# Optimization experiments

Hardware: AMD Instinct MI355X
Metric: run time of the kernel (lower is better)

## Reference

```python
import jax, jax.numpy as jnp
import numpy as np

L, B = 512, 1024
K = 64
IN, OBS, ST = 32, 32, 32


def setup_inputs() -> dict:
    key = jax.random.key(0)
    ks = iter(jax.random.split(key, 64))
    def W(o, i):
        return (jax.random.normal(next(ks), (o, i), jnp.float32) / np.sqrt(i)).astype(jnp.float32)
    def b(o):
        return (jax.random.normal(next(ks), (o,), jnp.float32) * 0.01).astype(jnp.float32)
    return dict(
        external_input_seq=jax.random.normal(next(ks), (L, B, IN), jnp.float32),
        observations_seq=jax.random.normal(next(ks), (L, B, OBS), jnp.float32),
        eps=jax.random.normal(next(ks), (L, B, ST), jnp.float32),
        pu_W1=W(K, IN), pu_b1=b(K), pu_W2=W(K, K), pu_b2=b(K),
        px_W1=W(K, OBS), px_b1=b(K), px_W2=W(K, K), px_b2=b(K),
        pz_W1=W(K, ST), pz_b1=b(K), pz_W2=W(K, K), pz_b2=b(K),
        post_W1=W(K, K), post_b1=b(K), post_W2=W(K, K), post_b2=b(K),
        post_Wmu=W(ST, K), post_bmu=b(ST), post_Wls=W(ST, K), post_bls=b(ST),
        inf_Wih=W(3 * K, K), inf_Whh=W(3 * K, K), inf_bih=b(3 * K), inf_bhh=b(3 * K),
        gen_Wih=W(3 * K, 2 * K), gen_Whh=W(3 * K, K), gen_bih=b(3 * K), gen_bhh=b(3 * K),
    )


def _preprocess(x, W1, b1, W2, b2):
    # PreProcess: two Linear+ReLU layers
    t = jax.nn.relu(x @ W1.T + b1)
    return jax.nn.relu(t @ W2.T + b2)


def _dblock(x, W1, b1, W2, b2, Wmu, bmu, Wls, bls):
    # DBlock_Relu: gated hidden t = relu(fc1(x)) * sigmoid(fc2(x)); heads mu, logsigma
    t = jax.nn.relu(x @ W1.T + b1) * jax.nn.sigmoid(x @ W2.T + b2)
    return x @ jnp.zeros((0,))[None, :0].T if False else (t @ Wmu.T + bmu, t @ Wls.T + bls)


def _gru(xs, h0, Wih, Whh, bih, bhh):
    # torch.nn.GRU gate order: reset, update, new
    def step(h, x):
        gi = x @ Wih.T + bih
        gh = h @ Whh.T + bhh
        i_r, i_z, i_n = jnp.split(gi, 3, axis=-1)
        h_r, h_z, h_n = jnp.split(gh, 3, axis=-1)
        r = jax.nn.sigmoid(i_r + h_r)
        z = jax.nn.sigmoid(i_z + h_z)
        n = jnp.tanh(i_n + r * h_n)
        h_new = (1.0 - z) * n + z * h
        return h_new, h_new
    return jax.lax.scan(step, h0, xs)


def reference(external_input_seq, observations_seq, eps,
              pu_W1, pu_b1, pu_W2, pu_b2,
              px_W1, px_b1, px_W2, px_b2,
              pz_W1, pz_b1, pz_W2, pz_b2,
              post_W1, post_b1, post_W2, post_b2,
              post_Wmu, post_bmu, post_Wls, post_bls,
              inf_Wih, inf_Whh, inf_bih, inf_bhh,
              gen_Wih, gen_Whh, gen_bih, gen_bhh):
    l, batch, _ = external_input_seq.shape
    k = inf_Whh.shape[1]
    h0 = jnp.zeros((batch, k), external_input_seq.dtype)

    u_emb = _preprocess(external_input_seq, pu_W1, pu_b1, pu_W2, pu_b2)   # [l,b,k]
    x_emb = _preprocess(observations_seq, px_W1, px_b1, px_W2, px_b2)     # [l,b,k]

    _, d_seq = _gru(x_emb, h0, inf_Wih, inf_Whh, inf_bih, inf_bhh)        # [l,b,k]

    # posterior q(z_t | d_t) — depends only on d_seq, so fully vectorized over time
    z_mu, z_logsigma = _dblock(d_seq, post_W1, post_b1, post_W2, post_b2,
                               post_Wmu, post_bmu, post_Wls, post_bls)
    sampled_state = z_mu + jnp.exp(0.5 * z_logsigma) * eps               # reparam sample

    z_emb = _preprocess(sampled_state, pz_W1, pz_b1, pz_W2, pz_b2)        # [l,b,k]
    gen_in = jnp.concatenate([z_emb, u_emb], axis=-1)                     # [l,b,2k]
    hn, h_all = _gru(gen_in, h0, gen_Wih, gen_Whh, gen_bih, gen_bhh)
    # h_seq in original is [h0, h1, ..., h_{l-1}] (drops last)
    h_seq = jnp.concatenate([h0[None], h_all[:-1]], axis=0)

    return (z_mu, z_logsigma, sampled_state, h_seq, x_emb, hn)
```

## Files before the change

kernel.cpp:

```cpp
#include <hip/hip_runtime.h>

#define L_T 512
#define BATCH 1024
#define LB (L_T*BATCH)
#define NT (LB/64)

typedef short bf16x8 __attribute__((ext_vector_type(8)));
typedef float f32x4 __attribute__((ext_vector_type(4)));
typedef unsigned short u16;

#define MFMA_B16(a,b,c) __builtin_amdgcn_mfma_f32_16x16x32_bf16((a),(b),(c),0,0,0)

__device__ __forceinline__ short f2bs(float f){
  union{float f; unsigned u;} c; c.f=f;
  unsigned r = (c.u + 0x7FFFu + ((c.u>>16)&1u)) >> 16;
  return (short)r;
}

__device__ __forceinline__ unsigned cvtpk(float lo, float hi){
  unsigned d;
  asm("v_cvt_pk_bf16_f32 %0, %1, %2" : "=v"(d) : "v"(lo), "v"(hi));
  return d;
}

__device__ __forceinline__ float fsig(float x){
  return __builtin_amdgcn_rcpf(1.0f + __expf(-x));
}
__device__ __forceinline__ float ftanh(float x){
  return 1.0f - 2.0f*__builtin_amdgcn_rcpf(1.0f + __expf(2.0f*x));
}

__device__ __forceinline__ void store8(u16* d, float4 a, float4 b){
  bf16x8 v;
  v[0]=f2bs(a.x); v[1]=f2bs(a.y); v[2]=f2bs(a.z); v[3]=f2bs(a.w);
  v[4]=f2bs(b.x); v[5]=f2bs(b.y); v[6]=f2bs(b.z); v[7]=f2bs(b.w);
  *(bf16x8*)d = v;
}

__device__ __forceinline__ bf16x8 bfrag_f32(const float* p){
  float4 a = *(const float4*)p;
  float4 b = *(const float4*)(p+4);
  bf16x8 v;
  v[0]=f2bs(a.x); v[1]=f2bs(a.y); v[2]=f2bs(a.z); v[3]=f2bs(a.w);
  v[4]=f2bs(b.x); v[5]=f2bs(b.y); v[6]=f2bs(b.z); v[7]=f2bs(b.w);
  return v;
}

__device__ __forceinline__ void dma16(const void* g, void* l){
  __builtin_amdgcn_global_load_lds(
      (const __attribute__((address_space(1))) void*)g,
      (__attribute__((address_space(3))) void*)l, 16, 0, 0);
}

__device__ __forceinline__ void pre_body(
    int bid,
    const float* __restrict__ src, const float* __restrict__ W1,
    const float* __restrict__ b1, const float* __restrict__ W2,
    const float* __restrict__ b2,
    u16* __restrict__ out_b16, int ostride, int ooff,
    float* __restrict__ out_f32)
{
  __shared__ u16 in_t[64*40];
  __shared__ u16 w1t[64*40];
  __shared__ u16 w2t[64*88];
  __shared__ u16 t1t[64*88];
  __shared__ float lb1[64], lb2[64];

  const int t = threadIdx.x;
  const size_t row0 = (size_t)bid * 64;

  {
    int r = t>>2, q = t&3;
    const float* ps = src + (row0 + r)*32 + q*8;
    store8(in_t + r*40 + q*8, *(const float4*)ps, *(const float4*)(ps+4));
    const float* pw = W1 + r*32 + q*8;
    store8(w1t + r*40 + q*8, *(const float4*)pw, *(const float4*)(pw+4));
    const float* pw2 = W2 + r*64 + q*16;
    store8(w2t + r*88 + q*16,     *(const float4*)pw2,     *(const float4*)(pw2+4));
    store8(w2t + r*88 + q*16 + 8, *(const float4*)(pw2+8), *(const float4*)(pw2+12));
    if (t < 64) lb1[t] = b1[t];
    else if (t < 128) lb2[t-64] = b2[t-64];
  }
  __syncthreads();

  const int lane = t & 63, wave = t >> 6;
  const int l15 = lane & 15, l4 = lane >> 4;
  const int rs = wave*16;

  {
    bf16x8 a = *(const bf16x8*)(in_t + (rs + l15)*40 + l4*8);
    #pragma unroll
    for (int ct = 0; ct < 4; ++ct) {
      f32x4 acc = {0.f,0.f,0.f,0.f};
      bf16x8 bw = *(const bf16x8*)(w1t + (ct*16 + l15)*40 + l4*8);
      acc = MFMA_B16(a, bw, acc);
      float bias = lb1[ct*16 + l15];
      #pragma unroll
      for (int i = 0; i < 4; ++i) {
        float v = fmaxf(acc[i] + bias, 0.f);
        t1t[(rs + l4*4 + i)*88 + ct*16 + l15] = (u16)f2bs(v);
      }
    }
  }
  __syncthreads();

  {
    bf16x8 a0 = *(const bf16x8*)(t1t + (rs + l15)*88 + l4*8);
    bf16x8 a1 = *(const bf16x8*)(t1t + (rs + l15)*88 + 32 + l4*8);
    #pragma unroll
    for (int ct = 0; ct < 4; ++ct) {
      f32x4 acc = {0.f,0.f,0.f,0.f};
      bf16x8 b0 = *(const bf16x8*)(w2t + (ct*16 + l15)*88 + l4*8);
      bf16x8 b1v = *(const bf16x8*)(w2t + (ct*16 + l15)*88 + 32 + l4*8);
      acc = MFMA_B16(a0, b0, acc);
      acc = MFMA_B16(a1, b1v, acc);
      float bias = lb2[ct*16 + l15];
      #pragma unroll
      for (int i = 0; i < 4; ++i) {
        float v = fmaxf(acc[i] + bias, 0.f);
        size_t gr = row0 + rs + l4*4 + i;
        int col = ct*16 + l15;
        if (out_b16) out_b16[gr*(size_t)ostride + ooff + col] = (u16)f2bs(v);
        if (out_f32) out_f32[gr*64 + col] = v;
      }
    }
  }
}

__global__ __launch_bounds__(256) void k_pre2(
    const float* __restrict__ obs,
    const float* __restrict__ pxW1, const float* __restrict__ pxb1,
    const float* __restrict__ pxW2, const float* __restrict__ pxb2,
    u16* __restrict__ xemb16, float* __restrict__ xembf32,
    const float* __restrict__ ext,
    const float* __restrict__ puW1, const float* __restrict__ pub1,
    const float* __restrict__ puW2, const float* __restrict__ pub2,
    u16* __restrict__ gen_in)
{
  int bid = blockIdx.x;
  if (bid < NT) pre_body(bid, obs, pxW1, pxb1, pxW2, pxb2, xemb16, 64, 0, xembf32);
  else          pre_body(bid - NT, ext, puW1, pub1, puW2, pub2, gen_in, 128, 64, nullptr);
}


#define SMEM_U16 39552
#define M_DT   0
#define M_W1T  5632
#define M_W2T  11264
#define M_TT   16896
#define M_ZW2T 22528
#define M_ZW1T 28160
#define M_ST   30720
#define M_WMUT 33280
#define M_WLST 36096
#define M_BIAS 38912

__device__ void inf_phase(
    int P, u16* smem,
    const u16* __restrict__ xin,
    const float* __restrict__ Wih, const float* __restrict__ Whh,
    const float* __restrict__ bih, const float* __restrict__ bhh,
    u16* __restrict__ dseq_out,
    float* __restrict__ hstate)
{
  u16* xchunk = smem;
  u16* ht     = smem + 16384;

  const int t = threadIdx.x;
  const int lane = t & 63, wave = t >> 6;
  const int l15 = lane & 15, l4 = lane >> 4;
  const int b0 = blockIdx.x * 16;
  const int kcol = wave*16 + l15;
  const int c0   = wave*16 + l4*4;

  bf16x8 wihf[3][2], whhf[3][2];
  #pragma unroll
  for (int g = 0; g < 3; ++g) {
    int grow = g*64 + kcol;
    #pragma unroll
    for (int kc = 0; kc < 2; ++kc) {
      wihf[g][kc] = bfrag_f32(Wih + (size_t)grow*64 + kc*32 + l4*8);
      whhf[g][kc] = bfrag_f32(Whh + (size_t)grow*64 + kc*32 + l4*8);
    }
  }
  f32x4 bv0, bv1, bvi, bvh;
  #pragma unroll
  for (int i = 0; i < 4; ++i) {
    bv0[i] = bih[c0+i]      + bhh[c0+i];
    bv1[i] = bih[64+c0+i]   + bhh[64+c0+i];
    bvi[i] = bih[128+c0+i];
    bvh[i] = bhh[128+c0+i];
  }

  auto issue_chunk = [&](int gc, int bufi){
    const size_t step0 = (size_t)gc*8;
    u16* dst0 = xchunk + bufi*8192;
    #pragma unroll
    for (int j = 0; j < 4; ++j) {
      int o = (j*4 + wave)*1024;
      int slot = o/16 + lane;
      int r_all = slot >> 3;
      int q = slot & 7;
      int slice = r_all >> 4, r = r_all & 15;
      int qs = q ^ (r & 7);
      const u16* g = xin + ((step0 + slice)*BATCH + b0 + r)*64 + qs*8;
      dma16(g, dst0 + o/2);
    }
  };

  float h[4];
  if (P == 0) { h[0]=h[1]=h[2]=h[3]=0.f; }
  else {
    float4 hv = *(const float4*)(hstate + (size_t)(b0 + l15)*64 + c0);
    h[0]=hv.x; h[1]=hv.y; h[2]=hv.z; h[3]=hv.w;
  }

  f32x4 gp0, gp1, gp2;
  issue_chunk(P*8, 0);

  for (int cc = 0; cc < 8; ++cc) {
    const int gc = P*8 + cc;
    const int cb = cc & 1;
    const u16* xbuf = xchunk + cb*8192;
    #pragma unroll
    for (int sp = 0; sp < 8; ++sp) {
      const int step = gc*8 + sp;

      {
        uint2 pv; pv.x = cvtpk(h[0], h[1]); pv.y = cvtpk(h[2], h[3]);
        *(uint2*)(ht + (sp&1)*1152 + l15*72 + c0) = pv;
      }

      if (sp == 0) asm volatile("s_waitcnt vmcnt(0)" ::: "memory");
      asm volatile("s_waitcnt lgkmcnt(0)\n\ts_barrier" ::: "memory");

      const u16* htr = ht + (sp&1)*1152 + l15*72;
      bf16x8 ha0 = *(const bf16x8*)(htr + l4*8);
      bf16x8 ha1 = *(const bf16x8*)(htr + 32 + l4*8);

      f32x4 a0, a1, a2;
      if (sp == 0) {
        const u16* xb = xbuf + l15*64;
        bf16x8 xa[2];
        #pragma unroll
        for (int kc = 0; kc < 2; ++kc)
          xa[kc] = *(const bf16x8*)(xb + (((l4 + 4*kc) ^ (l15 & 7)) * 8));
        a0 = bv0; a1 = bv1; a2 = bvi;
        #pragma unroll
        for (int kc = 0; kc < 2; ++kc) {
          a0 = MFMA_B16(wihf[0][kc], xa[kc], a0);
          a1 = MFMA_B16(wihf[1][kc], xa[kc], a1);
          a2 = MFMA_B16(wihf[2][kc], xa[kc], a2);
        }
      } else {
        a0 = gp0; a1 = gp1; a2 = gp2;
      }

      if (sp == 1 && cc + 1 < 8) issue_chunk(gc + 1, cb ^ 1);

      f32x4 g0 = MFMA_B16(whhf[0][0], ha0, a0);
      g0       = MFMA_B16(whhf[0][1], ha1, g0);
      f32x4 g1 = MFMA_B16(whhf[1][0], ha0, a1);
      g1       = MFMA_B16(whhf[1][1], ha1, g1);
      f32x4 gn = MFMA_B16(whhf[2][0], ha0, bvh);
      gn       = MFMA_B16(whhf[2][1], ha1, gn);

      if (sp < 7) {
        const u16* xb = xbuf + (sp+1)*1024 + l15*64;
        bf16x8 xn[2];
        #pragma unroll
        for (int kc = 0; kc < 2; ++kc)
          xn[kc] = *(const bf16x8*)(xb + (((l4 + 4*kc) ^ (l15 & 7)) * 8));
        gp0 = bv0; gp1 = bv1; gp2 = bvi;
        #pragma unroll
        for (int kc = 0; kc < 2; ++kc) {
          gp0 = MFMA_B16(wihf[0][kc], xn[kc], gp0);
          gp1 = MFMA_B16(wihf[1][kc], xn[kc], gp1);
          gp2 = MFMA_B16(wihf[2][kc], xn[kc], gp2);
        }
      }

      #pragma unroll
      for (int i = 0; i < 4; ++i) {
        float r = fsig(g0[i]);
        float z = fsig(g1[i]);
        float n = ftanh(a2[i] + r*gn[i]);
        h[i] = z*(h[i] - n) + n;
      }

      {
        uint2 dv; dv.x = cvtpk(h[0], h[1]); dv.y = cvtpk(h[2], h[3]);
        *(uint2*)(dseq_out + ((size_t)step*BATCH + b0 + l15)*64 + c0) = dv;
      }
    }
  }

  float4 hv; hv.x=h[0]; hv.y=h[1]; hv.z=h[2]; hv.w=h[3];
  *(float4*)(hstate + (size_t)(b0 + l15)*64 + c0) = hv;
}

__device__ void gen_phase(
    int P, u16* smem,
    const u16* __restrict__ xin,
    const float* __restrict__ Wih, const float* __restrict__ Whh,
    const float* __restrict__ bih, const float* __restrict__ bhh,
    float* __restrict__ hseq,
    float* __restrict__ hstate)
{
  u16* xchunk = smem;
  u16* ht     = smem + 32768;

  const int t = threadIdx.x;
  const int lane = t & 63, wave = t >> 6;
  const int l15 = lane & 15, l4 = lane >> 4;
  const int b0 = (blockIdx.x - 64) * 16;
  const int kcol = wave*16 + l15;
  const int c0   = wave*16 + l4*4;

  bf16x8 wihf[3][4], whhf[3][2];
  #pragma unroll
  for (int g = 0; g < 3; ++g) {
    int grow = g*64 + kcol;
    #pragma unroll
    for (int kc = 0; kc < 4; ++kc)
      wihf[g][kc] = bfrag_f32(Wih + (size_t)grow*128 + kc*32 + l4*8);
    #pragma unroll
    for (int kc = 0; kc < 2; ++kc)
      whhf[g][kc] = bfrag_f32(Whh + (size_t)grow*64 + kc*32 + l4*8);
  }
  f32x4 bv0, bv1, bvi, bvh;
  #pragma unroll
  for (int i = 0; i < 4; ++i) {
    bv0[i] = bih[c0+i]      + bhh[c0+i];
    bv1[i] = bih[64+c0+i]   + bhh[64+c0+i];
    bvi[i] = bih[128+c0+i];
    bvh[i] = bhh[128+c0+i];
  }

  auto issue_chunk = [&](int gc, int bufi){
    const size_t step0 = (size_t)gc*8;
    u16* dst0 = xchunk + bufi*16384;
    #pragma unroll
    for (int j = 0; j < 8; ++j) {
      int o = (j*4 + wave)*1024;
      int slot = o/16 + lane;
      int r_all = slot >> 4;
      int q = slot & 15;
      int slice = r_all >> 4, r = r_all & 15;
      int qs = q ^ (r & 7);
      const u16* g = xin + ((step0 + slice)*BATCH + b0 + r)*128 + qs*8;
      dma16(g, dst0 + o/2);
    }
  };

  float h[4];
  if (P == 2) { h[0]=h[1]=h[2]=h[3]=0.f; }
  else {
    float4 hv = *(const float4*)(hstate + (size_t)(b0 + l15)*64 + c0);
    h[0]=hv.x; h[1]=hv.y; h[2]=hv.z; h[3]=hv.w;
  }

  const int C0 = (P - 2) * 8;
  f32x4 gp0, gp1, gp2;
  issue_chunk(C0, 0);

  for (int cc = 0; cc < 8; ++cc) {
    const int gc = C0 + cc;
    const int cb = cc & 1;
    const u16* xbuf = xchunk + cb*16384;
    #pragma unroll
    for (int sp = 0; sp < 8; ++sp) {
      const int step = gc*8 + sp;

      {
        uint2 pv; pv.x = cvtpk(h[0], h[1]); pv.y = cvtpk(h[2], h[3]);
        *(uint2*)(ht + (sp&1)*1152 + l15*72 + c0) = pv;
        float4 hv; hv.x=h[0]; hv.y=h[1]; hv.z=h[2]; hv.w=h[3];
        *(float4*)(hseq + ((size_t)step*BATCH + b0 + l15)*64 + c0) = hv;
      }

      if (sp == 0) asm volatile("s_waitcnt vmcnt(0)" ::: "memory");
      asm volatile("s_waitcnt lgkmcnt(0)\n\ts_barrier" ::: "memory");

      const u16* htr = ht + (sp&1)*1152 + l15*72;
      bf16x8 ha0 = *(const bf16x8*)(htr + l4*8);
      bf16x8 ha1 = *(const bf16x8*)(htr + 32 + l4*8);

      f32x4 a0, a1, a2;
      if (sp == 0) {
        const u16* xb = xbuf + l15*128;
        bf16x8 xa[4];
        #pragma unroll
        for (int kc = 0; kc < 4; ++kc)
          xa[kc] = *(const bf16x8*)(xb + (((l4 + 4*kc) ^ (l15 & 7)) * 8));
        a0 = bv0; a1 = bv1; a2 = bvi;
        #pragma unroll
        for (int kc = 0; kc < 4; ++kc) {
          a0 = MFMA_B16(wihf[0][kc], xa[kc], a0);
          a1 = MFMA_B16(wihf[1][kc], xa[kc], a1);
          a2 = MFMA_B16(wihf[2][kc], xa[kc], a2);
        }
      } else {
        a0 = gp0; a1 = gp1; a2 = gp2;
      }

      if (sp == 1 && cc + 1 < 8) issue_chunk(gc + 1, cb ^ 1);

      f32x4 g0 = MFMA_B16(whhf[0][0], ha0, a0);
      g0       = MFMA_B16(whhf[0][1], ha1, g0);
      f32x4 g1 = MFMA_B16(whhf[1][0], ha0, a1);
      g1       = MFMA_B16(whhf[1][1], ha1, g1);
      f32x4 gn = MFMA_B16(whhf[2][0], ha0, bvh);
      gn       = MFMA_B16(whhf[2][1], ha1, gn);

      if (sp < 7) {
        const u16* xb = xbuf + (sp+1)*2048 + l15*128;
        bf16x8 xn[4];
        #pragma unroll
        for (int kc = 0; kc < 4; ++kc)
          xn[kc] = *(const bf16x8*)(xb + (((l4 + 4*kc) ^ (l15 & 7)) * 8));
        gp0 = bv0; gp1 = bv1; gp2 = bvi;
        #pragma unroll
        for (int kc = 0; kc < 4; ++kc) {
          gp0 = MFMA_B16(wihf[0][kc], xn[kc], gp0);
          gp1 = MFMA_B16(wihf[1][kc], xn[kc], gp1);
          gp2 = MFMA_B16(wihf[2][kc], xn[kc], gp2);
        }
      }

      #pragma unroll
      for (int i = 0; i < 4; ++i) {
        float r = fsig(g0[i]);
        float z = fsig(g1[i]);
        float n = ftanh(a2[i] + r*gn[i]);
        h[i] = z*(h[i] - n) + n;
      }
    }
  }

  float4 hv; hv.x=h[0]; hv.y=h[1]; hv.z=h[2]; hv.w=h[3];
  *(float4*)(hstate + (size_t)(b0 + l15)*64 + c0) = hv;
}

__device__ void mid_phase(
    int P, u16* smem,
    const u16* __restrict__ dseq,
    const float* __restrict__ eps,
    const float* __restrict__ W1, const float* __restrict__ b1,
    const float* __restrict__ W2, const float* __restrict__ b2,
    const float* __restrict__ Wmu, const float* __restrict__ bmu,
    const float* __restrict__ Wls, const float* __restrict__ bls,
    const float* __restrict__ zW1, const float* __restrict__ zb1,
    const float* __restrict__ zW2, const float* __restrict__ zb2,
    float* __restrict__ out_mu, float* __restrict__ out_ls, float* __restrict__ out_s,
    u16* __restrict__ gen_in)
{
  u16* dt   = smem + M_DT;
  u16* w1t  = smem + M_W1T;
  u16* w2t  = smem + M_W2T;
  u16* tt   = smem + M_TT;
  u16* zw2t = smem + M_ZW2T;
  u16* zw1t = smem + M_ZW1T;
  u16* st   = smem + M_ST;
  u16* wmut = smem + M_WMUT;
  u16* wlst = smem + M_WLST;
  float* fb = (float*)(smem + M_BIAS);
  float* lb1 = fb, *lb2 = fb+64, *lbz1 = fb+128, *lbz2 = fb+192;
  float* lbmu = fb+256, *lbls = fb+288;

  const int t = threadIdx.x;

  {
    int r = t>>2, q = t&3;
    const float* p1 = W1 + r*64 + q*16;
    store8(w1t + r*88 + q*16,     *(const float4*)p1,     *(const float4*)(p1+4));
    store8(w1t + r*88 + q*16 + 8, *(const float4*)(p1+8), *(const float4*)(p1+12));
    const float* p2 = W2 + r*64 + q*16;
    store8(w2t + r*88 + q*16,     *(const float4*)p2,     *(const float4*)(p2+4));
    store8(w2t + r*88 + q*16 + 8, *(const float4*)(p2+8), *(const float4*)(p2+12));
    const float* pz2 = zW2 + r*64 + q*16;
    store8(zw2t + r*88 + q*16,     *(const float4*)pz2,     *(const float4*)(pz2+4));
    store8(zw2t + r*88 + q*16 + 8, *(const float4*)(pz2+8), *(const float4*)(pz2+12));
    const float* pz1 = zW1 + r*32 + q*8;
    store8(zw1t + r*40 + q*8, *(const float4*)pz1, *(const float4*)(pz1+4));
    if (t < 128) {
      int r2 = t>>2, q2 = t&3;
      const float* pm = Wmu + r2*64 + q2*16;
      store8(wmut + r2*88 + q2*16,     *(const float4*)pm,     *(const float4*)(pm+4));
      store8(wmut + r2*88 + q2*16 + 8, *(const float4*)(pm+8), *(const float4*)(pm+12));
    } else {
      int t2 = t - 128; int r2 = t2>>2, q2 = t2&3;
      const float* pl = Wls + r2*64 + q2*16;
      store8(wlst + r2*88 + q2*16,     *(const float4*)pl,     *(const float4*)(pl+4));
      store8(wlst + r2*88 + q2*16 + 8, *(const float4*)(pl+8), *(const float4*)(pl+12));
    }
    if (t < 64) { lb1[t] = b1[t]; lbz1[t] = zb1[t]; }
    else if (t < 128) { lb2[t-64] = b2[t-64]; lbz2[t-64] = zb2[t-64]; }
    else if (t < 160) lbmu[t-128] = bmu[t-128];
    else if (t < 192) lbls[t-160] = bls[t-160];
  }

  const int lane = t & 63, wave = t >> 6;
  const int l15 = lane & 15, l4 = lane >> 4;
  const int rs = wave*16;
  const int bidm = blockIdx.x - 128;
  const size_t t0 = (size_t)(P - 1) * 64;

  for (int j = 0; j < 8; ++j) {
    const size_t row0 = t0*BATCH + ((size_t)bidm*8 + j)*64;

    __syncthreads();
    {
      int r = t>>2, q = t&3;
      const u16* pd = dseq + (row0 + r)*64 + q*16;
      *(bf16x8*)(dt + r*88 + q*16)     = *(const bf16x8*)pd;
      *(bf16x8*)(dt + r*88 + q*16 + 8) = *(const bf16x8*)(pd + 8);
    }
    __syncthreads();

    {
      bf16x8 a0 = *(const bf16x8*)(dt + (rs + l15)*88 + l4*8);
      bf16x8 a1 = *(const bf16x8*)(dt + (rs + l15)*88 + 32 + l4*8);
      #pragma unroll
      for (int ct = 0; ct < 4; ++ct) {
        f32x4 c1 = {0.f,0.f,0.f,0.f}, c2 = {0.f,0.f,0.f,0.f};
        bf16x8 w1a = *(const bf16x8*)(w1t + (ct*16 + l15)*88 + l4*8);
        bf16x8 w1b = *(const bf16x8*)(w1t + (ct*16 + l15)*88 + 32 + l4*8);
        bf16x8 w2a = *(const bf16x8*)(w2t + (ct*16 + l15)*88 + l4*8);
        bf16x8 w2b = *(const bf16x8*)(w2t + (ct*16 + l15)*88 + 32 + l4*8);
        c1 = MFMA_B16(a0, w1a, c1); c1 = MFMA_B16(a1, w1b, c1);
        c2 = MFMA_B16(a0, w2a, c2); c2 = MFMA_B16(a1, w2b, c2);
        float bb1 = lb1[ct*16 + l15], bb2 = lb2[ct*16 + l15];
        #pragma unroll
        for (int i = 0; i < 4; ++i) {
          float tv = fmaxf(c1[i] + bb1, 0.f) * fsig(c2[i] + bb2);
          tt[(rs + l4*4 + i)*88 + ct*16 + l15] = (u16)f2bs(tv);
        }
      }
    }
    __syncthreads();

    {
      bf16x8 a0 = *(const bf16x8*)(tt + (rs + l15)*88 + l4*8);
      bf16x8 a1 = *(const bf16x8*)(tt + (rs + l15)*88 + 32 + l4*8);
      #pragma unroll
      for (int ct = 0; ct < 2; ++ct) {
        f32x4 cmu = {0.f,0.f,0.f,0.f}, cls = {0.f,0.f,0.f,0.f};
        bf16x8 wma = *(const bf16x8*)(wmut + (ct*16 + l15)*88 + l4*8);
        bf16x8 wmb = *(const bf16x8*)(wmut + (ct*16 + l15)*88 + 32 + l4*8);
        bf16x8 wla = *(const bf16x8*)(wlst + (ct*16 + l15)*88 + l4*8);
        bf16x8 wlb = *(const bf16x8*)(wlst + (ct*16 + l15)*88 + 32 + l4*8);
        cmu = MFMA_B16(a0, wma, cmu); cmu = MFMA_B16(a1, wmb, cmu);
        cls = MFMA_B16(a0, wla, cls); cls = MFMA_B16(a1, wlb, cls);
        float bm = lbmu[ct*16 + l15], bl = lbls[ct*16 + l15];
        #pragma unroll
        for (int i = 0; i < 4; ++i) {
          size_t R = row0 + rs + l4*4 + i;
          int col = ct*16 + l15;
          float mu = cmu[i] + bm;
          float ls = cls[i] + bl;
          float e  = eps[R*32 + col];
          float s  = mu + __expf(0.5f*ls)*e;
          out_mu[R*32 + col] = mu;
          out_ls[R*32 + col] = ls;
          out_s [R*32 + col] = s;
          st[(rs + l4*4 + i)*40 + col] = (u16)f2bs(s);
        }
      }
    }
    __syncthreads();

    {
      bf16x8 a = *(const bf16x8*)(st + (rs + l15)*40 + l4*8);
      #pragma unroll
      for (int ct = 0; ct < 4; ++ct) {
        f32x4 acc = {0.f,0.f,0.f,0.f};
        bf16x8 bw = *(const bf16x8*)(zw1t + (ct*16 + l15)*40 + l4*8);
        acc = MFMA_B16(a, bw, acc);
        float bias = lbz1[ct*16 + l15];
        #pragma unroll
        for (int i = 0; i < 4; ++i) {
          float v = fmaxf(acc[i] + bias, 0.f);
          dt[(rs + l4*4 + i)*88 + ct*16 + l15] = (u16)f2bs(v);
        }
      }
    }
    __syncthreads();

    {
      bf16x8 a0 = *(const bf16x8*)(dt + (rs + l15)*88 + l4*8);
      bf16x8 a1 = *(const bf16x8*)(dt + (rs + l15)*88 + 32 + l4*8);
      #pragma unroll
      for (int ct = 0; ct < 4; ++ct) {
        f32x4 acc = {0.f,0.f,0.f,0.f};
        bf16x8 b0 = *(const bf16x8*)(zw2t + (ct*16 + l15)*88 + l4*8);
        bf16x8 b1v = *(const bf16x8*)(zw2t + (ct*16 + l15)*88 + 32 + l4*8);
        acc = MFMA_B16(a0, b0, acc);
        acc = MFMA_B16(a1, b1v, acc);
        float bias = lbz2[ct*16 + l15];
        #pragma unroll
        for (int i = 0; i < 4; ++i) {
          float v = fmaxf(acc[i] + bias, 0.f);
          size_t gr = row0 + rs + l4*4 + i;
          gen_in[gr*128 + ct*16 + l15] = (u16)f2bs(v);
        }
      }
    }
  }
}

__global__ __launch_bounds__(256, 1) void k_phase(
    int P,
    const u16* xemb16, u16* gen_in,
    const float* eps,
    const float* iWih, const float* iWhh, const float* ibih, const float* ibhh,
    const float* gWih, const float* gWhh, const float* gbih, const float* gbhh,
    const float* poW1, const float* pob1, const float* poW2, const float* pob2,
    const float* poWmu, const float* pobmu, const float* poWls, const float* pobls,
    const float* pzW1, const float* pzb1, const float* pzW2, const float* pzb2,
    u16* dseq, float* out_mu, float* out_ls, float* out_s,
    float* hseq, float* hn, float* hstate_inf)
{
  __shared__ u16 smem[SMEM_U16];
  const int bid = blockIdx.x;
  if (bid < 64) {
    if (P < 8)
      inf_phase(P, smem, xemb16, iWih, iWhh, ibih, ibhh, dseq, hstate_inf);
  } else if (bid < 128) {
    if (P >= 2)
      gen_phase(P, smem, gen_in, gWih, gWhh, gbih, gbhh, hseq, hn);
  } else {
    if (P >= 1 && P <= 8)
      mid_phase(P, smem, dseq, eps, poW1, pob1, poW2, pob2,
                poWmu, pobmu, poWls, pobls, pzW1, pzb1, pzW2, pzb2,
                out_mu, out_ls, out_s, gen_in);
  }
}


extern "C" void kernel_launch(void* const* d_in, const int* in_sizes, int n_in,
                              void* d_out, int out_size, void* d_ws, size_t ws_size,
                              hipStream_t stream) {
  const float* ext  = (const float*)d_in[0];
  const float* obs  = (const float*)d_in[1];
  const float* eps  = (const float*)d_in[2];
  const float* puW1 = (const float*)d_in[3];  const float* pub1 = (const float*)d_in[4];
  const float* puW2 = (const float*)d_in[5];  const float* pub2 = (const float*)d_in[6];
  const float* pxW1 = (const float*)d_in[7];  const float* pxb1 = (const float*)d_in[8];
  const float* pxW2 = (const float*)d_in[9];  const float* pxb2 = (const float*)d_in[10];
  const float* pzW1 = (const float*)d_in[11]; const float* pzb1 = (const float*)d_in[12];
  const float* pzW2 = (const float*)d_in[13]; const float* pzb2 = (const float*)d_in[14];
  const float* poW1 = (const float*)d_in[15]; const float* pob1 = (const float*)d_in[16];
  const float* poW2 = (const float*)d_in[17]; const float* pob2 = (const float*)d_in[18];
  const float* poWmu= (const float*)d_in[19]; const float* pobmu= (const float*)d_in[20];
  const float* poWls= (const float*)d_in[21]; const float* pobls= (const float*)d_in[22];
  const float* iWih = (const float*)d_in[23]; const float* iWhh = (const float*)d_in[24];
  const float* ibih = (const float*)d_in[25]; const float* ibhh = (const float*)d_in[26];
  const float* gWih = (const float*)d_in[27]; const float* gWhh = (const float*)d_in[28];
  const float* gbih = (const float*)d_in[29]; const float* gbhh = (const float*)d_in[30];

  float* out = (float*)d_out;
  const size_t OFF_MU   = 0;
  const size_t OFF_LS   = (size_t)LB*32;
  const size_t OFF_S    = (size_t)LB*64;
  const size_t OFF_HSEQ = (size_t)LB*96;
  const size_t OFF_XEMB = (size_t)LB*96 + (size_t)LB*64;
  const size_t OFF_HN   = OFF_XEMB + (size_t)LB*64;

  u16* gen_in = (u16*)d_ws;
  u16* dseq   = (u16*)(out + OFF_MU);
  u16* xemb16 = (u16*)(out + OFF_HSEQ + (size_t)LB*32);
  float* hstate_inf = out + OFF_S + (size_t)LB*32 - 65536;

  k_pre2<<<2*NT, 256, 0, stream>>>(obs, pxW1, pxb1, pxW2, pxb2, xemb16, out + OFF_XEMB,
                                   ext, puW1, pub1, puW2, pub2, gen_in);
  for (int P = 0; P < 10; ++P) {
    k_phase<<<256, 256, 0, stream>>>(P, xemb16, gen_in, eps,
                                     iWih, iWhh, ibih, ibhh,
                                     gWih, gWhh, gbih, gbhh,
                                     poW1, pob1, poW2, pob2,
                                     poWmu, pobmu, poWls, pobls,
                                     pzW1, pzb1, pzW2, pzb2,
                                     dseq, out + OFF_MU, out + OFF_LS, out + OFF_S,
                                     out + OFF_HSEQ, out + OFF_HN, hstate_inf);
  }
}
```

Measured before the change: 485.3 us.

## Overlap input preprocessing with recurrent phases by deferring tiles to mid blocks

```diff
diff --git a/kernel.cpp b/kernel.cpp
--- a/kernel.cpp
+++ b/kernel.cpp
@@ -52,22 +52,40 @@
       (__attribute__((address_space(3))) void*)l, 16, 0, 0);
 }
 
-__device__ __forceinline__ void pre_body(
-    int bid,
+#define SMEM_U16 39552
+#define M_DT   0
+#define M_W1T  5632
+#define M_W2T  11264
+#define M_TT   16896
+#define M_ZW2T 22528
+#define M_ZW1T 28160
+#define M_ST   30720
+#define M_WMUT 33280
+#define M_WLST 36096
+#define M_BIAS 38912
+#define PT_IN   0
+#define PT_W1   2560
+#define PT_W2   5120
+#define PT_T1   10752
+#define PT_BIAS 16384
+
+__device__ void pre_tile(
+    u16* smem, size_t row0,
     const float* __restrict__ src, const float* __restrict__ W1,
     const float* __restrict__ b1, const float* __restrict__ W2,
     const float* __restrict__ b2,
     u16* __restrict__ out_b16, int ostride, int ooff,
     float* __restrict__ out_f32)
 {
-  __shared__ u16 in_t[64*40];
-  __shared__ u16 w1t[64*40];
-  __shared__ u16 w2t[64*88];
-  __shared__ u16 t1t[64*88];
-  __shared__ float lb1[64], lb2[64];
+  u16* in_t = smem + PT_IN;
+  u16* w1t  = smem + PT_W1;
+  u16* w2t  = smem + PT_W2;
+  u16* t1t  = smem + PT_T1;
+  float* lb1 = (float*)(smem + PT_BIAS);
+  float* lb2 = lb1 + 64;
 
   const int t = threadIdx.x;
-  const size_t row0 = (size_t)bid * 64;
+  __syncthreads();
 
   {
     int r = t>>2, q = t&3;
@@ -120,14 +138,14 @@
         float v = fmaxf(acc[i] + bias, 0.f);
         size_t gr = row0 + rs + l4*4 + i;
         int col = ct*16 + l15;
-        if (out_b16) out_b16[gr*(size_t)ostride + ooff + col] = (u16)f2bs(v);
+        out_b16[gr*(size_t)ostride + ooff + col] = (u16)f2bs(v);
         if (out_f32) out_f32[gr*64 + col] = v;
       }
     }
   }
 }
 
-__global__ __launch_bounds__(256) void k_pre2(
+__global__ __launch_bounds__(256) void k_pre_small(
     const float* __restrict__ obs,
     const float* __restrict__ pxW1, const float* __restrict__ pxb1,
     const float* __restrict__ pxW2, const float* __restrict__ pxb2,
@@ -137,23 +155,16 @@
     const float* __restrict__ puW2, const float* __restrict__ pub2,
     u16* __restrict__ gen_in)
 {
+  __shared__ u16 smem[16640];
   int bid = blockIdx.x;
-  if (bid < NT) pre_body(bid, obs, pxW1, pxb1, pxW2, pxb2, xemb16, 64, 0, xembf32);
-  else          pre_body(bid - NT, ext, puW1, pub1, puW2, pub2, gen_in, 128, 64, nullptr);
-}
-
-
-#define SMEM_U16 39552
-#define M_DT   0
-#define M_W1T  5632
-#define M_W2T  11264
-#define M_TT   16896
-#define M_ZW2T 22528
-#define M_ZW1T 28160
-#define M_ST   30720
-#define M_WMUT 33280
-#define M_WLST 36096
-#define M_BIAS 38912
+  if (bid < 2048)
+    pre_tile(smem, (size_t)bid*64, obs, pxW1, pxb1, pxW2, pxb2,
+             xemb16, 64, 0, xembf32);
+  else
+    pre_tile(smem, (size_t)(bid-2048)*64, ext, puW1, pub1, puW2, pub2,
+             gen_in, 128, 64, nullptr);
+}
+
 
 __device__ void inf_phase(
     int P, u16* smem,
@@ -453,165 +464,189 @@
     const float* __restrict__ zW1, const float* __restrict__ zb1,
     const float* __restrict__ zW2, const float* __restrict__ zb2,
     float* __restrict__ out_mu, float* __restrict__ out_ls, float* __restrict__ out_s,
-    u16* __restrict__ gen_in)
+    u16* __restrict__ gen_in,
+    const float* __restrict__ obs,
+    const float* __restrict__ pxW1, const float* __restrict__ pxb1,
+    const float* __restrict__ pxW2, const float* __restrict__ pxb2,
+    u16* __restrict__ xemb16, float* __restrict__ xembf32,
+    const float* __restrict__ ext,
+    const float* __restrict__ puW1, const float* __restrict__ pub1,
+    const float* __restrict__ puW2, const float* __restrict__ pub2)
 {
-  u16* dt   = smem + M_DT;
-  u16* w1t  = smem + M_W1T;
-  u16* w2t  = smem + M_W2T;
-  u16* tt   = smem + M_TT;
-  u16* zw2t = smem + M_ZW2T;
-  u16* zw1t = smem + M_ZW1T;
-  u16* st   = smem + M_ST;
-  u16* wmut = smem + M_WMUT;
-  u16* wlst = smem + M_WLST;
-  float* fb = (float*)(smem + M_BIAS);
-  float* lb1 = fb, *lb2 = fb+64, *lbz1 = fb+128, *lbz2 = fb+192;
-  float* lbmu = fb+256, *lbls = fb+288;
-
   const int t = threadIdx.x;
-
-  {
-    int r = t>>2, q = t&3;
-    const float* p1 = W1 + r*64 + q*16;
-    store8(w1t + r*88 + q*16,     *(const float4*)p1,     *(const float4*)(p1+4));
-    store8(w1t + r*88 + q*16 + 8, *(const float4*)(p1+8), *(const float4*)(p1+12));
-    const float* p2 = W2 + r*64 + q*16;
-    store8(w2t + r*88 + q*16,     *(const float4*)p2,     *(const float4*)(p2+4));
-    store8(w2t + r*88 + q*16 + 8, *(const float4*)(p2+8), *(const float4*)(p2+12));
-    const float* pz2 = zW2 + r*64 + q*16;
-    store8(zw2t + r*88 + q*16,     *(const float4*)pz2,     *(const float4*)(pz2+4));
-    store8(zw2t + r*88 + q*16 + 8, *(const float4*)(pz2+8), *(const float4*)(pz2+12));
-    const float* pz1 = zW1 + r*32 + q*8;
-    store8(zw1t + r*40 + q*8, *(const float4*)pz1, *(const float4*)(pz1+4));
-    if (t < 128) {
-      int r2 = t>>2, q2 = t&3;
-      const float* pm = Wmu + r2*64 + q2*16;
-      store8(wmut + r2*88 + q2*16,     *(const float4*)pm,     *(const float4*)(pm+4));
-      store8(wmut + r2*88 + q2*16 + 8, *(const float4*)(pm+8), *(const float4*)(pm+12));
-    } else {
-      int t2 = t - 128; int r2 = t2>>2, q2 = t2&3;
-      const float* pl = Wls + r2*64 + q2*16;
-      store8(wlst + r2*88 + q2*16,     *(const float4*)pl,     *(const float4*)(pl+4));
-      store8(wlst + r2*88 + q2*16 + 8, *(const float4*)(pl+8), *(const float4*)(pl+12));
-    }
-    if (t < 64) { lb1[t] = b1[t]; lbz1[t] = zb1[t]; }
-    else if (t < 128) { lb2[t-64] = b2[t-64]; lbz2[t-64] = zb2[t-64]; }
-    else if (t < 160) lbmu[t-128] = bmu[t-128];
-    else if (t < 192) lbls[t-160] = bls[t-160];
-  }
-
-  const int lane = t & 63, wave = t >> 6;
-  const int l15 = lane & 15, l4 = lane >> 4;
-  const int rs = wave*16;
   const int bidm = blockIdx.x - 128;
-  const size_t t0 = (size_t)(P - 1) * 64;
-
-  for (int j = 0; j < 8; ++j) {
-    const size_t row0 = t0*BATCH + ((size_t)bidm*8 + j)*64;
-
-    __syncthreads();
+
+  if (P >= 1 && P <= 8) {
+    u16* dt   = smem + M_DT;
+    u16* w1t  = smem + M_W1T;
+    u16* w2t  = smem + M_W2T;
+    u16* tt   = smem + M_TT;
+    u16* zw2t = smem + M_ZW2T;
+    u16* zw1t = smem + M_ZW1T;
+    u16* st   = smem + M_ST;
+    u16* wmut = smem + M_WMUT;
+    u16* wlst = smem + M_WLST;
+    float* fb = (float*)(smem + M_BIAS);
+    float* lb1 = fb, *lb2 = fb+64, *lbz1 = fb+128, *lbz2 = fb+192;
+    float* lbmu = fb+256, *lbls = fb+288;
+
     {
       int r = t>>2, q = t&3;
-      const u16* pd = dseq + (row0 + r)*64 + q*16;
-      *(bf16x8*)(dt + r*88 + q*16)     = *(const bf16x8*)pd;
-      *(bf16x8*)(dt + r*88 + q*16 + 8) = *(const bf16x8*)(pd + 8);
-    }
-    __syncthreads();
-
-    {
-      bf16x8 a0 = *(const bf16x8*)(dt + (rs + l15)*88 + l4*8);
-      bf16x8 a1 = *(const bf16x8*)(dt + (rs + l15)*88 + 32 + l4*8);
-      #pragma unroll
-      for (int ct = 0; ct < 4; ++ct) {
-        f32x4 c1 = {0.f,0.f,0.f,0.f}, c2 = {0.f,0.f,0.f,0.f};
-        bf16x8 w1a = *(const bf16x8*)(w1t + (ct*16 + l15)*88 + l4*8);
-        bf16x8 w1b = *(const bf16x8*)(w1t + (ct*16 + l15)*88 + 32 + l4*8);
-        bf16x8 w2a = *(const bf16x8*)(w2t + (ct*16 + l15)*88 + l4*8);
-        bf16x8 w2b = *(const bf16x8*)(w2t + (ct*16 + l15)*88 + 32 + l4*8);
-        c1 = MFMA_B16(a0, w1a, c1); c1 = MFMA_B16(a1, w1b, c1);
-        c2 = MFMA_B16(a0, w2a, c2); c2 = MFMA_B16(a1, w2b, c2);
-        float bb1 = lb1[ct*16 + l15], bb2 = lb2[ct*16 + l15];
-        #pragma unroll
-        for (int i = 0; i < 4; ++i) {
-          float tv = fmaxf(c1[i] + bb1, 0.f) * fsig(c2[i] + bb2);
-          tt[(rs + l4*4 + i)*88 + ct*16 + l15] = (u16)f2bs(tv);
+      const float* p1 = W1 + r*64 + q*16;
+      store8(w1t + r*88 + q*16,     *(const float4*)p1,     *(const float4*)(p1+4));
+      store8(w1t + r*88 + q*16 + 8, *(const float4*)(p1+8), *(const float4*)(p1+12));
+      const float* p2 = W2 + r*64 + q*16;
+      store8(w2t + r*88 + q*16,     *(const float4*)p2,     *(const float4*)(p2+4));
+      store8(w2t + r*88 + q*16 + 8, *(const float4*)(p2+8), *(const float4*)(p2+12));
+      const float* pz2 = zW2 + r*64 + q*16;
+      store8(zw2t + r*88 + q*16,     *(const float4*)pz2,     *(const float4*)(pz2+4));
+      store8(zw2t + r*88 + q*16 + 8, *(const float4*)(pz2+8), *(const float4*)(pz2+12));
+      const float* pz1 = zW1 + r*32 + q*8;
+      store8(zw1t + r*40 + q*8, *(const float4*)pz1, *(const float4*)(pz1+4));
+      if (t < 128) {
+        int r2 = t>>2, q2 = t&3;
+        const float* pm = Wmu + r2*64 + q2*16;
+        store8(wmut + r2*88 + q2*16,     *(const float4*)pm,     *(const float4*)(pm+4));
+        store8(wmut + r2*88 + q2*16 + 8, *(const float4*)(pm+8), *(const float4*)(pm+12));
+      } else {
+        int t2 = t - 128; int r2 = t2>>2, q2 = t2&3;
+        const float* pl = Wls + r2*64 + q2*16;
+        store8(wlst + r2*88 + q2*16,     *(const float4*)pl,     *(const float4*)(pl+4));
+        store8(wlst + r2*88 + q2*16 + 8, *(const float4*)(pl+8), *(const float4*)(pl+12));
+      }
+      if (t < 64) { lb1[t] = b1[t]; lbz1[t] = zb1[t]; }
+      else if (t < 128) { lb2[t-64] = b2[t-64]; lbz2[t-64] = zb2[t-64]; }
+      else if (t < 160) lbmu[t-128] = bmu[t-128];
+      else if (t < 192) lbls[t-160] = bls[t-160];
+    }
+
+    const int lane = t & 63, wave = t >> 6;
+    const int l15 = lane & 15, l4 = lane >> 4;
+    const int rs = wave*16;
+    const size_t t0 = (size_t)(P - 1) * 64;
+
+    for (int j = 0; j < 8; ++j) {
+      const size_t row0 = t0*BATCH + ((size_t)bidm*8 + j)*64;
+
+      __syncthreads();
+      {
+        int r = t>>2, q = t&3;
+        const u16* pd = dseq + (row0 + r)*64 + q*16;
+        *(bf16x8*)(dt + r*88 + q*16)     = *(const bf16x8*)pd;
+        *(bf16x8*)(dt + r*88 + q*16 + 8) = *(const bf16x8*)(pd + 8);
+      }
+      __syncthreads();
+
+      {
+        bf16x8 a0 = *(const bf16x8*)(dt + (rs + l15)*88 + l4*8);
+        bf16x8 a1 = *(const bf16x8*)(dt + (rs + l15)*88 + 32 + l4*8);
+        #pragma unroll
+        for (int ct = 0; ct < 4; ++ct) {
+          f32x4 c1 = {0.f,0.f,0.f,0.f}, c2 = {0.f,0.f,0.f,0.f};
+          bf16x8 w1a = *(const bf16x8*)(w1t + (ct*16 + l15)*88 + l4*8);
+          bf16x8 w1b = *(const bf16x8*)(w1t + (ct*16 + l15)*88 + 32 + l4*8);
+          bf16x8 w2a = *(const bf16x8*)(w2t + (ct*16 + l15)*88 + l4*8);
+          bf16x8 w2b = *(const bf16x8*)(w2t + (ct*16 + l15)*88 + 32 + l4*8);
+          c1 = MFMA_B16(a0, w1a, c1); c1 = MFMA_B16(a1, w1b, c1);
+          c2 = MFMA_B16(a0, w2a, c2); c2 = MFMA_B16(a1, w2b, c2);
+          float bb1 = lb1[ct*16 + l15], bb2 = lb2[ct*16 + l15];
+          #pragma unroll
+          for (int i = 0; i < 4; ++i) {
+            float tv = fmaxf(c1[i] + bb1, 0.f) * fsig(c2[i] + bb2);
+            tt[(rs + l4*4 + i)*88 + ct*16 + l15] = (u16)f2bs(tv);
+          }
         }
       }
-    }
-    __syncthreads();
-
-    {
-      bf16x8 a0 = *(const bf16x8*)(tt + (rs + l15)*88 + l4*8);
-      bf16x8 a1 = *(const bf16x8*)(tt + (rs + l15)*88 + 32 + l4*8);
-      #pragma unroll
-      for (int ct = 0; ct < 2; ++ct) {
-        f32x4 cmu = {0.f,0.f,0.f,0.f}, cls = {0.f,0.f,0.f,0.f};
-        bf16x8 wma = *(const bf16x8*)(wmut + (ct*16 + l15)*88 + l4*8);
-        bf16x8 wmb = *(const bf16x8*)(wmut + (ct*16 + l15)*88 + 32 + l4*8);
-        bf16x8 wla = *(const bf16x8*)(wlst + (ct*16 + l15)*88 + l4*8);
-        bf16x8 wlb = *(const bf16x8*)(wlst + (ct*16 + l15)*88 + 32 + l4*8);
-        cmu = MFMA_B16(a0, wma, cmu); cmu = MFMA_B16(a1, wmb, cmu);
-        cls = MFMA_B16(a0, wla, cls); cls = MFMA_B16(a1, wlb, cls);
-        float bm = lbmu[ct*16 + l15], bl = lbls[ct*16 + l15];
-        #pragma unroll
-        for (int i = 0; i < 4; ++i) {
-          size_t R = row0 + rs + l4*4 + i;
-          int col = ct*16 + l15;
-          float mu = cmu[i] + bm;
-          float ls = cls[i] + bl;
-          float e  = eps[R*32 + col];
-          float s  = mu + __expf(0.5f*ls)*e;
-          out_mu[R*32 + col] = mu;
-          out_ls[R*32 + col] = ls;
-          out_s [R*32 + col] = s;
-          st[(rs + l4*4 + i)*40 + col] = (u16)f2bs(s);
+      __syncthreads();
+
+      {
+        bf16x8 a0 = *(const bf16x8*)(tt + (rs + l15)*88 + l4*8);
+        bf16x8 a1 = *(const bf16x8*)(tt + (rs + l15)*88 + 32 + l4*8);
+        #pragma unroll
+        for (int ct = 0; ct < 2; ++ct) {
+          f32x4 cmu = {0.f,0.f,0.f,0.f}, cls = {0.f,0.f,0.f,0.f};
+          bf16x8 wma = *(const bf16x8*)(wmut + (ct*16 + l15)*88 + l4*8);
+          bf16x8 wmb = *(const bf16x8*)(wmut + (ct*16 + l15)*88 + 32 + l4*8);
+          bf16x8 wla = *(const bf16x8*)(wlst + (ct*16 + l15)*88 + l4*8);
+          bf16x8 wlb = *(const bf16x8*)(wlst + (ct*16 + l15)*88 + 32 + l4*8);
+          cmu = MFMA_B16(a0, wma, cmu); cmu = MFMA_B16(a1, wmb, cmu);
+          cls = MFMA_B16(a0, wla, cls); cls = MFMA_B16(a1, wlb, cls);
+          float bm = lbmu[ct*16 + l15], bl = lbls[ct*16 + l15];
+          #pragma unroll
+          for (int i = 0; i < 4; ++i) {
+            size_t R = row0 + rs + l4*4 + i;
+            int col = ct*16 + l15;
+            float mu = cmu[i] + bm;
+            float ls = cls[i] + bl;
+            float e  = eps[R*32 + col];
+            float s  = mu + __expf(0.5f*ls)*e;
+            out_mu[R*32 + col] = mu;
+            out_ls[R*32 + col] = ls;
+            out_s [R*32 + col] = s;
+            st[(rs + l4*4 + i)*40 + col] = (u16)f2bs(s);
+          }
         }
       }
-    }
-    __syncthreads();
-
-    {
-      bf16x8 a = *(const bf16x8*)(st + (rs + l15)*40 + l4*8);
-      #pragma unroll
-      for (int ct = 0; ct < 4; ++ct) {
-        f32x4 acc = {0.f,0.f,0.f,0.f};
-        bf16x8 bw = *(const bf16x8*)(zw1t + (ct*16 + l15)*40 + l4*8);
-        acc = MFMA_B16(a, bw, acc);
-        float bias = lbz1[ct*16 + l15];
-        #pragma unroll
-        for (int i = 0; i < 4; ++i) {
-          float v = fmaxf(acc[i] + bias, 0.f);
-          dt[(rs + l4*4 + i)*88 + ct*16 + l15] = (u16)f2bs(v);
+      __syncthreads();
+
+      {
+        bf16x8 a = *(const bf16x8*)(st + (rs + l15)*40 + l4*8);
+        #pragma unroll
+        for (int ct = 0; ct < 4; ++ct) {
+          f32x4 acc = {0.f,0.f,0.f,0.f};
+          bf16x8 bw = *(const bf16x8*)(zw1t + (ct*16 + l15)*40 + l4*8);
+          acc = MFMA_B16(a, bw, acc);
+          float bias = lbz1[ct*16 + l15];
+          #pragma unroll
+          for (int i = 0; i < 4; ++i) {
+            float v = fmaxf(acc[i] + bias, 0.f);
+            dt[(rs + l4*4 + i)*88 + ct*16 + l15] = (u16)f2bs(v);
+          }
         }
       }
-    }
-    __syncthreads();
-
-    {
-      bf16x8 a0 = *(const bf16x8*)(dt + (rs + l15)*88 + l4*8);
-      bf16x8 a1 = *(const bf16x8*)(dt + (rs + l15)*88 + 32 + l4*8);
-      #pragma unroll
-      for (int ct = 0; ct < 4; ++ct) {
-        f32x4 acc = {0.f,0.f,0.f,0.f};
-        bf16x8 b0 = *(const bf16x8*)(zw2t + (ct*16 + l15)*88 + l4*8);
-        bf16x8 b1v = *(const bf16x8*)(zw2t + (ct*16 + l15)*88 + 32 + l4*8);
-        acc = MFMA_B16(a0, b0, acc);
-        acc = MFMA_B16(a1, b1v, acc);
-        float bias = lbz2[ct*16 + l15];
-        #pragma unroll
-        for (int i = 0; i < 4; ++i) {
-          float v = fmaxf(acc[i] + bias, 0.f);
-          size_t gr = row0 + rs + l4*4 + i;
-          gen_in[gr*128 + ct*16 + l15] = (u16)f2bs(v);
+      __syncthreads();
+
+      {
+        bf16x8 a0 = *(const bf16x8*)(dt + (rs + l15)*88 + l4*8);
+        bf16x8 a1 = *(const bf16x8*)(dt + (rs + l15)*88 + 32 + l4*8);
+        #pragma unroll
+        for (int ct = 0; ct < 4; ++ct) {
+          f32x4 acc = {0.f,0.f,0.f,0.f};
+          bf16x8 b0 = *(const bf16x8*)(zw2t + (ct*16 + l15)*88 + l4*8);
+          bf16x8 b1v = *(const bf16x8*)(zw2t + (ct*16 + l15)*88 + 32 + l4*8);
+          acc = MFMA_B16(a0, b0, acc);
+          acc = MFMA_B16(a1, b1v, acc);
+          float bias = lbz2[ct*16 + l15];
+          #pragma unroll
+          for (int i = 0; i < 4; ++i) {
+            float v = fmaxf(acc[i] + bias, 0.f);
+            size_t gr = row0 + rs + l4*4 + i;
+            gen_in[gr*128 + ct*16 + l15] = (u16)f2bs(v);
+          }
         }
       }
+    }
+  }
+
+  if (P <= 5) {
+    for (int k = 0; k < 8; ++k) {
+      size_t tile = (size_t)(P+2)*1024 + (size_t)bidm*8 + k;
+      pre_tile(smem, tile*64, obs, pxW1, pxb1, pxW2, pxb2,
+               xemb16, 64, 0, xembf32);
+    }
+  }
+  if (P <= 6) {
+    for (int k = 0; k < 8; ++k) {
+      size_t tile = (size_t)(P+1)*1024 + (size_t)bidm*8 + k;
+      pre_tile(smem, tile*64, ext, puW1, pub1, puW2, pub2,
+               gen_in, 128, 64, nullptr);
     }
   }
 }
 
 __global__ __launch_bounds__(256, 1) void k_phase(
     int P,
-    const u16* xemb16, u16* gen_in,
+    const u16* xemb16_c, u16* gen_in,
     const float* eps,
     const float* iWih, const float* iWhh, const float* ibih, const float* ibhh,
     const float* gWih, const float* gWhh, const float* gbih, const float* gbhh,
@@ -619,21 +654,27 @@
     const float* poWmu, const float* pobmu, const float* poWls, const float* pobls,
     const float* pzW1, const float* pzb1, const float* pzW2, const float* pzb2,
     u16* dseq, float* out_mu, float* out_ls, float* out_s,
-    float* hseq, float* hn, float* hstate_inf)
+    float* hseq, float* hn, float* hstate_inf,
+    const float* obs,
+    const float* pxW1, const float* pxb1, const float* pxW2, const float* pxb2,
+    u16* xemb16_w, float* xembf32,
+    const float* ext,
+    const float* puW1, const float* pub1, const float* puW2, const float* pub2)
 {
   __shared__ u16 smem[SMEM_U16];
   const int bid = blockIdx.x;
   if (bid < 64) {
     if (P < 8)
-      inf_phase(P, smem, xemb16, iWih, iWhh, ibih, ibhh, dseq, hstate_inf);
+      inf_phase(P, smem, xemb16_c, iWih, iWhh, ibih, ibhh, dseq, hstate_inf);
   } else if (bid < 128) {
     if (P >= 2)
       gen_phase(P, smem, gen_in, gWih, gWhh, gbih, gbhh, hseq, hn);
   } else {
-    if (P >= 1 && P <= 8)
-      mid_phase(P, smem, dseq, eps, poW1, pob1, poW2, pob2,
-                poWmu, pobmu, poWls, pobls, pzW1, pzb1, pzW2, pzb2,
-                out_mu, out_ls, out_s, gen_in);
+    mid_phase(P, smem, dseq, eps, poW1, pob1, poW2, pob2,
+              poWmu, pobmu, poWls, pobls, pzW1, pzb1, pzW2, pzb2,
+              out_mu, out_ls, out_s, gen_in,
+              obs, pxW1, pxb1, pxW2, pxb2, xemb16_w, xembf32,
+              ext, puW1, pub1, puW2, pub2);
   }
 }
 
@@ -672,8 +713,9 @@
   u16* xemb16 = (u16*)(out + OFF_HSEQ + (size_t)LB*32);
   float* hstate_inf = out + OFF_S + (size_t)LB*32 - 65536;
 
-  k_pre2<<<2*NT, 256, 0, stream>>>(obs, pxW1, pxb1, pxW2, pxb2, xemb16, out + OFF_XEMB,
-                                   ext, puW1, pub1, puW2, pub2, gen_in);
+  k_pre_small<<<3072, 256, 0, stream>>>(obs, pxW1, pxb1, pxW2, pxb2,
+                                        xemb16, out + OFF_XEMB,
+                                        ext, puW1, pub1, puW2, pub2, gen_in);
   for (int P = 0; P < 10; ++P) {
     k_phase<<<256, 256, 0, stream>>>(P, xemb16, gen_in, eps,
                                      iWih, iWhh, ibih, ibhh,
@@ -682,6 +724,9 @@
                                      poWmu, pobmu, poWls, pobls,
                                      pzW1, pzb1, pzW2, pzb2,
                                      dseq, out + OFF_MU, out + OFF_LS, out + OFF_S,
-                                     out + OFF_HSEQ, out + OFF_HN, hstate_inf);
-  }
-}
+                                     out + OFF_HSEQ, out + OFF_HN, hstate_inf,
+                                     obs, pxW1, pxb1, pxW2, pxb2,
+                                     xemb16, out + OFF_XEMB,
+                                     ext, puW1, pub1, puW2, pub2);
+  }
+}
```

New measurement: 704.1 us. 45.1% more time.
